# Kernel optimization log

Measured on AMD Instinct MI355X. Metric: run time of the kernel, lower is better.

Reference implementation:

```python
import jax, jax.numpy as jnp
import numpy as np

Nknn = 10
Np = 20
N = 524288
DOWN, LEFT, RIGHT, UP, WIDTH = -5.0, -5.0, 5.0, 5.0, 1.0


def setup_inputs() -> dict:
    key = jax.random.key(0)
    ks = jax.random.split(key, 20)
    def p(k, shape, fan_in):
        return jax.random.normal(k, shape, jnp.float32) / jnp.sqrt(jnp.float32(fan_in))
    inp = {
        "t": jax.random.uniform(ks[0], (1,), jnp.float32),
        "y": jax.random.normal(ks[1], (N, 4 + 2 * Np), jnp.float32),
        # net1: Linear(4,8) -> ReLU -> Linear(8,2)
        "w1a": p(ks[2], (4, 8), 4),   "b1a": p(ks[3], (8,), 4),
        "w1b": p(ks[4], (8, 2), 8),   "b1b": p(ks[5], (2,), 8),
        # net2: Linear(1,16) -> ReLU -> Linear(16,8) -> ReLU -> Linear(8,1)
        "w2a": p(ks[6], (1, 16), 1),  "b2a": p(ks[7], (16,), 1),
        "w2b": p(ks[8], (16, 8), 16), "b2b": p(ks[9], (8,), 16),
        "w2c": p(ks[10], (8, 1), 8),  "b2c": p(ks[11], (1,), 8),
        # net3: same architecture as net2
        "w3a": p(ks[12], (1, 16), 1), "b3a": p(ks[13], (16,), 1),
        "w3b": p(ks[14], (16, 8), 16),"b3b": p(ks[15], (8,), 16),
        "w3c": p(ks[16], (8, 1), 8),  "b3c": p(ks[17], (1,), 8),
    }
    return inp


def _mlp3(x, wa, ba, wb, bb, wc, bc):
    # Linear -> ReLU -> Linear -> ReLU -> Linear, applied on last axis
    h = jax.nn.relu(x @ wa + ba)
    h = jax.nn.relu(h @ wb + bb)
    return h @ wc + bc


def reference(t, y, w1a, b1a, w1b, b1b, w2a, b2a, w2b, b2b, w2c, b2c,
              w3a, b3a, w3b, b3b, w3c, b3c):
    y = y.astype(jnp.float32)
    theX = y[:, 0:2]            # positions [N,2]
    theV = y[:, 2:4]            # velocities [N,2]
    ux = y[:, 4:4 + 2 * Nknn].reshape(-1, Nknn, 2)  # neighbor offsets [N,Nknn,2]

    dxdt = theV

    # goal-attraction term f1
    door = jnp.array([RIGHT + 0.6, 0.0], jnp.float32)
    diff = door - theX
    unit_e = diff / jnp.sqrt(jnp.sum(diff * diff, axis=1, keepdims=True))
    h = jax.nn.relu(jnp.concatenate([unit_e, theV], axis=1) @ w1a + b1a)
    f1 = h @ w1b + b1b          # [N,2]

    # wall-repulsion term f2; rows inside the door gap get rightdist=100
    x0 = theX[:, 0:1]
    x1 = theX[:, 1:2]
    rightdist = jnp.where((x1 < WIDTH) & (x1 > -WIDTH), 100.0, RIGHT - x0)
    wall_in = jnp.stack([x0 - LEFT, x1 - DOWN, UP - x1, rightdist], axis=1)  # [N,4,1]
    o = _mlp3(wall_in, w2a, b2a, w2b, bb=b2b, wc=w2c, bc=b2c) if False else _mlp3(wall_in, w2a, b2a, w2b, b2b, w2c, b2c)  # [N,4,1]
    # directions: [1,0], [0,1], [0,-1], [-1,0]
    f2 = jnp.concatenate([o[:, 0] - o[:, 3], o[:, 1] - o[:, 2]], axis=1)  # [N,2]

    # neighbor-repulsion term f3 (vectorized over Nknn)
    d = jnp.sqrt(jnp.sum(ux * ux, axis=2, keepdims=True))  # [N,Nknn,1]
    f3 = -jnp.sum(_mlp3(d, w3a, b3a, w3b, b3b, w3c, b3c) * ux / d, axis=1)  # [N,2]

    dvdt = (f1 + f2 + f3) / 80.0
    dudt = jnp.zeros((y.shape[0], 2 * Nknn), y.dtype)
    result = jnp.concatenate([dxdt, dvdt, dudt], axis=1)  # [N, 4 + 2*Nknn]

    # zero out agents that have exited (x > RIGHT)
    result = jnp.where((theX[:, 0] > RIGHT)[:, None], 0.0, result)
    return result
```

## Files before the change

### kernel.cpp

```cpp
#include <hip/hip_runtime.h>

#define NROW  524288
#define BLK   256
#define NKNN  10
#define YCOLS 44
#define OCOLS 24

#define TBL    256
#define T2_LO  (-2.0f)
#define T3_LO  (0.0f)
#define T_H    (1.0f / 16.0f)
#define T_INVH 16.0f

typedef float f32x4 __attribute__((ext_vector_type(4)));

__device__ __forceinline__ float mlp_scalar_g(float s,
    const float* __restrict__ wa, const float* __restrict__ ba,
    const float* __restrict__ wb, const float* __restrict__ bb,
    const float* __restrict__ wc, const float* __restrict__ bc) {
    float h[16];
#pragma unroll
    for (int j = 0; j < 16; ++j)
        h[j] = fmaxf(fmaf(s, wa[j], ba[j]), 0.0f);
    float g[8];
#pragma unroll
    for (int k = 0; k < 8; ++k) g[k] = bb[k];
#pragma unroll
    for (int j = 0; j < 16; ++j) {
        float hj = h[j];
#pragma unroll
        for (int k = 0; k < 8; ++k)
            g[k] = fmaf(hj, wb[j * 8 + k], g[k]);
    }
    float o = bc[0];
#pragma unroll
    for (int k = 0; k < 8; ++k)
        o = fmaf(fmaxf(g[k], 0.0f), wc[k], o);
    return o;
}

__device__ __forceinline__ float tbl_eval(const float* __restrict__ T, float s, float lo) {
    float u = (s - lo) * T_INVH;
    u = fminf(fmaxf(u, 0.0f), (float)TBL - 1.001f);
    int i = (int)u;
    float f = u - (float)i;
    float va = T[i];
    float vb = T[i + 1];
    return fmaf(f, vb - va, va);
}

__global__ __launch_bounds__(BLK) void odefunc_kernel(
    const float* __restrict__ y,
    const float* __restrict__ w1a, const float* __restrict__ b1a,
    const float* __restrict__ w1b, const float* __restrict__ b1b,
    const float* __restrict__ w2a, const float* __restrict__ b2a,
    const float* __restrict__ w2b, const float* __restrict__ b2b,
    const float* __restrict__ w2c, const float* __restrict__ b2c,
    const float* __restrict__ w3a, const float* __restrict__ b3a,
    const float* __restrict__ w3b, const float* __restrict__ b3b,
    const float* __restrict__ w3c, const float* __restrict__ b3c,
    float* __restrict__ out)
{
    __shared__ f32x4 S[BLK * 6];
    __shared__ float T2v[TBL];
    __shared__ float T3v[TBL];
    __shared__ float o100s;

    const int t    = threadIdx.x;
    const int w    = t >> 6;
    const int lane = t & 63;

    const f32x4* yb = reinterpret_cast<const f32x4*>(y) + (size_t)blockIdx.x * BLK * (YCOLS / 4);
    f32x4 ld[6];
    int jj[6];
#pragma unroll
    for (int i = 0; i < 6; ++i) {
        int j  = lane + i * 64;
        int rr = j / 6;
        int cc = j - rr * 6;
        jj[i]  = j;
        ld[i]  = yb[(64 * w + rr) * 11 + cc];
    }

    T2v[t] = mlp_scalar_g(T2_LO + (float)t * T_H, w2a, b2a, w2b, b2b, w2c, b2c);
    T3v[t] = mlp_scalar_g(T3_LO + (float)t * T_H, w3a, b3a, w3b, b3b, w3c, b3c);
    if (t == 0)
        o100s = mlp_scalar_g(100.0f, w2a, b2a, w2b, b2b, w2c, b2c);

    __syncthreads();

#pragma unroll
    for (int i = 0; i < 6; ++i)
        S[384 * w + jj[i]] = ld[i];
    __builtin_amdgcn_wave_barrier();

    f32x4 a  = S[t * 6 + 0];
    f32x4 u0 = S[t * 6 + 1];
    f32x4 u1 = S[t * 6 + 2];
    f32x4 u2 = S[t * 6 + 3];
    f32x4 u3 = S[t * 6 + 4];
    f32x4 u4 = S[t * 6 + 5];
    const float o100 = o100s;

    float dx = 5.6f - a.x;
    float dy = 0.0f - a.y;
    float inv = rsqrtf(fmaf(dx, dx, dy * dy));
    float in1[4] = { dx * inv, dy * inv, a.z, a.w };
    float h1[8];
#pragma unroll
    for (int j = 0; j < 8; ++j) {
        float s = b1a[j];
#pragma unroll
        for (int k = 0; k < 4; ++k)
            s = fmaf(in1[k], w1a[k * 8 + j], s);
        h1[j] = fmaxf(s, 0.0f);
    }
    float f1x = b1b[0];
    float f1y = b1b[1];
#pragma unroll
    for (int j = 0; j < 8; ++j) {
        f1x = fmaf(h1[j], w1b[j * 2 + 0], f1x);
        f1y = fmaf(h1[j], w1b[j * 2 + 1], f1y);
    }

    bool corridor = (a.y < 1.0f) && (a.y > -1.0f);
    float o0 = tbl_eval(T2v, a.x + 5.0f, T2_LO);
    float o1 = tbl_eval(T2v, a.y + 5.0f, T2_LO);
    float o2 = tbl_eval(T2v, 5.0f - a.y, T2_LO);
    float o3 = corridor ? o100 : tbl_eval(T2v, 5.0f - a.x, T2_LO);
    float f2x = o0 - o3;
    float f2y = o1 - o2;

    float us[2 * NKNN] = { u0.x, u0.y, u0.z, u0.w,
                           u1.x, u1.y, u1.z, u1.w,
                           u2.x, u2.y, u2.z, u2.w,
                           u3.x, u3.y, u3.z, u3.w,
                           u4.x, u4.y, u4.z, u4.w };
    float f3x = 0.0f, f3y = 0.0f;
#pragma unroll
    for (int n = 0; n < NKNN; ++n) {
        float uxn = us[2 * n + 0];
        float uyn = us[2 * n + 1];
        float s2  = fmaf(uxn, uxn, uyn * uyn);
        float idn = rsqrtf(s2);
        float d   = s2 * idn;
        float m   = tbl_eval(T3v, d, T3_LO);
        float c   = m * idn;
        f3x = fmaf(-c, uxn, f3x);
        f3y = fmaf(-c, uyn, f3y);
    }

    bool dead = (a.x > 5.0f);
    const float k80 = 1.0f / 80.0f;
    f32x4 r;
    r.x = dead ? 0.0f : a.z;
    r.y = dead ? 0.0f : a.w;
    r.z = dead ? 0.0f : (f1x + f2x + f3x) * k80;
    r.w = dead ? 0.0f : (f1y + f2y + f3y) * k80;

    const f32x4 z = (f32x4)(0.0f);
    S[t * 6 + 0] = r;
    S[t * 6 + 1] = z;
    S[t * 6 + 2] = z;
    S[t * 6 + 3] = z;
    S[t * 6 + 4] = z;
    S[t * 6 + 5] = z;
    __builtin_amdgcn_wave_barrier();

    f32x4* o4 = reinterpret_cast<f32x4*>(out) + (size_t)blockIdx.x * BLK * (OCOLS / 4);
#pragma unroll
    for (int i = 0; i < 6; ++i) {
        int j = 384 * w + lane + i * 64;
        f32x4 v = S[j];
        __builtin_nontemporal_store(v, &o4[j]);
    }
}

extern "C" void kernel_launch(void* const* d_in, const int* in_sizes, int n_in,
                              void* d_out, int out_size, void* d_ws, size_t ws_size,
                              hipStream_t stream) {
    int iy = 1;
    for (int i = 0; i < n_in; ++i) {
        if (in_sizes[i] == NROW * YCOLS) { iy = i; break; }
    }
    const float* y   = (const float*)d_in[iy];
    const float* w1a = (const float*)d_in[iy + 1];
    const float* b1a = (const float*)d_in[iy + 2];
    const float* w1b = (const float*)d_in[iy + 3];
    const float* b1b = (const float*)d_in[iy + 4];
    const float* w2a = (const float*)d_in[iy + 5];
    const float* b2a = (const float*)d_in[iy + 6];
    const float* w2b = (const float*)d_in[iy + 7];
    const float* b2b = (const float*)d_in[iy + 8];
    const float* w2c = (const float*)d_in[iy + 9];
    const float* b2c = (const float*)d_in[iy + 10];
    const float* w3a = (const float*)d_in[iy + 11];
    const float* b3a = (const float*)d_in[iy + 12];
    const float* w3b = (const float*)d_in[iy + 13];
    const float* b3b = (const float*)d_in[iy + 14];
    const float* w3c = (const float*)d_in[iy + 15];
    const float* b3c = (const float*)d_in[iy + 16];
    float* out = (float*)d_out;

    hipLaunchKernelGGL(odefunc_kernel, dim3(NROW / BLK), dim3(BLK), 0, stream,
                       y, w1a, b1a, w1b, b1b,
                       w2a, b2a, w2b, b2b, w2c, b2c,
                       w3a, b3a, w3b, b3b, w3c, b3c, out);
}
```

Measured before the change: 30.48 us.

## Process two row tiles per block and prefetch the second during compute

Each block now handles two 256-row tiles instead of one, halving the grid. The per-block table build (two MLP lookup tables plus the o100 value) is amortized over twice as many rows. The second tile's global load is issued before computing the first tile, overlapping memory latency with compute. The cost is fewer blocks in flight and more registers held for the prefetched tile, which may reduce occupancy.

```diff
diff --git a/kernel.cpp b/kernel.cpp
--- a/kernel.cpp
+++ b/kernel.cpp
@@ -2,6 +2,7 @@
 
 #define NROW  524288
 #define BLK   256
+#define TPB   2
 #define NKNN  10
 #define YCOLS 44
 #define OCOLS 24
@@ -47,6 +48,112 @@
     float va = T[i];
     float vb = T[i + 1];
     return fmaf(f, vb - va, va);
+}
+
+__device__ __forceinline__ void load_tile(const f32x4* __restrict__ yb,
+                                          int w, int lane, f32x4 ld[6]) {
+#pragma unroll
+    for (int i = 0; i < 6; ++i) {
+        int j  = lane + i * 64;
+        int rr = j / 6;
+        int cc = j - rr * 6;
+        ld[i]  = yb[(64 * w + rr) * 11 + cc];
+    }
+}
+
+__device__ __forceinline__ void stage_tile(f32x4* __restrict__ S,
+                                           int w, int lane, const f32x4 ld[6]) {
+#pragma unroll
+    for (int i = 0; i < 6; ++i)
+        S[384 * w + lane + i * 64] = ld[i];
+}
+
+__device__ __forceinline__ void compute_row(f32x4* __restrict__ S, int t,
+    const float* __restrict__ T2v, const float* __restrict__ T3v, float o100,
+    const float* __restrict__ w1a, const float* __restrict__ b1a,
+    const float* __restrict__ w1b, const float* __restrict__ b1b)
+{
+    f32x4 a  = S[t * 6 + 0];
+    f32x4 u0 = S[t * 6 + 1];
+    f32x4 u1 = S[t * 6 + 2];
+    f32x4 u2 = S[t * 6 + 3];
+    f32x4 u3 = S[t * 6 + 4];
+    f32x4 u4 = S[t * 6 + 5];
+
+    float dx = 5.6f - a.x;
+    float dy = 0.0f - a.y;
+    float inv = rsqrtf(fmaf(dx, dx, dy * dy));
+    float in1[4] = { dx * inv, dy * inv, a.z, a.w };
+    float h1[8];
+#pragma unroll
+    for (int j = 0; j < 8; ++j) {
+        float s = b1a[j];
+#pragma unroll
+        for (int k = 0; k < 4; ++k)
+            s = fmaf(in1[k], w1a[k * 8 + j], s);
+        h1[j] = fmaxf(s, 0.0f);
+    }
+    float f1x = b1b[0];
+    float f1y = b1b[1];
+#pragma unroll
+    for (int j = 0; j < 8; ++j) {
+        f1x = fmaf(h1[j], w1b[j * 2 + 0], f1x);
+        f1y = fmaf(h1[j], w1b[j * 2 + 1], f1y);
+    }
+
+    bool corridor = (a.y < 1.0f) && (a.y > -1.0f);
+    float o0 = tbl_eval(T2v, a.x + 5.0f, T2_LO);
+    float o1 = tbl_eval(T2v, a.y + 5.0f, T2_LO);
+    float o2 = tbl_eval(T2v, 5.0f - a.y, T2_LO);
+    float o3 = corridor ? o100 : tbl_eval(T2v, 5.0f - a.x, T2_LO);
+    float f2x = o0 - o3;
+    float f2y = o1 - o2;
+
+    float us[2 * NKNN] = { u0.x, u0.y, u0.z, u0.w,
+                           u1.x, u1.y, u1.z, u1.w,
+                           u2.x, u2.y, u2.z, u2.w,
+                           u3.x, u3.y, u3.z, u3.w,
+                           u4.x, u4.y, u4.z, u4.w };
+    float f3x = 0.0f, f3y = 0.0f;
+#pragma unroll
+    for (int n = 0; n < NKNN; ++n) {
+        float uxn = us[2 * n + 0];
+        float uyn = us[2 * n + 1];
+        float s2  = fmaf(uxn, uxn, uyn * uyn);
+        float idn = rsqrtf(s2);
+        float d   = s2 * idn;
+        float m   = tbl_eval(T3v, d, T3_LO);
+        float c   = m * idn;
+        f3x = fmaf(-c, uxn, f3x);
+        f3y = fmaf(-c, uyn, f3y);
+    }
+
+    bool dead = (a.x > 5.0f);
+    const float k80 = 1.0f / 80.0f;
+    f32x4 r;
+    r.x = dead ? 0.0f : a.z;
+    r.y = dead ? 0.0f : a.w;
+    r.z = dead ? 0.0f : (f1x + f2x + f3x) * k80;
+    r.w = dead ? 0.0f : (f1y + f2y + f3y) * k80;
+
+    const f32x4 z = (f32x4)(0.0f);
+    S[t * 6 + 0] = r;
+    S[t * 6 + 1] = z;
+    S[t * 6 + 2] = z;
+    S[t * 6 + 3] = z;
+    S[t * 6 + 4] = z;
+    S[t * 6 + 5] = z;
+}
+
+__device__ __forceinline__ void store_tile(f32x4* __restrict__ ob,
+                                           const f32x4* __restrict__ S,
+                                           int w, int lane) {
+#pragma unroll
+    for (int i = 0; i < 6; ++i) {
+        int j = 384 * w + lane + i * 64;
+        f32x4 v = S[j];
+        __builtin_nontemporal_store(v, &ob[j]);
+    }
 }
 
 __global__ __launch_bounds__(BLK) void odefunc_kernel(
@@ -70,17 +177,15 @@
     const int w    = t >> 6;
     const int lane = t & 63;
 
-    const f32x4* yb = reinterpret_cast<const f32x4*>(y) + (size_t)blockIdx.x * BLK * (YCOLS / 4);
-    f32x4 ld[6];
-    int jj[6];
-#pragma unroll
-    for (int i = 0; i < 6; ++i) {
-        int j  = lane + i * 64;
-        int rr = j / 6;
-        int cc = j - rr * 6;
-        jj[i]  = j;
-        ld[i]  = yb[(64 * w + rr) * 11 + cc];
-    }
+    const f32x4* yb0 = reinterpret_cast<const f32x4*>(y)
+                     + (size_t)blockIdx.x * TPB * BLK * (YCOLS / 4);
+    const f32x4* yb1 = yb0 + BLK * (YCOLS / 4);
+    f32x4* ob0 = reinterpret_cast<f32x4*>(out)
+               + (size_t)blockIdx.x * TPB * BLK * (OCOLS / 4);
+    f32x4* ob1 = ob0 + BLK * (OCOLS / 4);
+
+    f32x4 ld0[6];
+    load_tile(yb0, w, lane, ld0);
 
     T2v[t] = mlp_scalar_g(T2_LO + (float)t * T_H, w2a, b2a, w2b, b2b, w2c, b2c);
     T3v[t] = mlp_scalar_g(T3_LO + (float)t * T_H, w3a, b3a, w3b, b3b, w3c, b3c);
@@ -88,92 +193,25 @@
         o100s = mlp_scalar_g(100.0f, w2a, b2a, w2b, b2b, w2c, b2c);
 
     __syncthreads();
-
-#pragma unroll
-    for (int i = 0; i < 6; ++i)
-        S[384 * w + jj[i]] = ld[i];
-    __builtin_amdgcn_wave_barrier();
-
-    f32x4 a  = S[t * 6 + 0];
-    f32x4 u0 = S[t * 6 + 1];
-    f32x4 u1 = S[t * 6 + 2];
-    f32x4 u2 = S[t * 6 + 3];
-    f32x4 u3 = S[t * 6 + 4];
-    f32x4 u4 = S[t * 6 + 5];
     const float o100 = o100s;
 
-    float dx = 5.6f - a.x;
-    float dy = 0.0f - a.y;
-    float inv = rsqrtf(fmaf(dx, dx, dy * dy));
-    float in1[4] = { dx * inv, dy * inv, a.z, a.w };
-    float h1[8];
-#pragma unroll
-    for (int j = 0; j < 8; ++j) {
-        float s = b1a[j];
-#pragma unroll
-        for (int k = 0; k < 4; ++k)
-            s = fmaf(in1[k], w1a[k * 8 + j], s);
-        h1[j] = fmaxf(s, 0.0f);
-    }
-    float f1x = b1b[0];
-    float f1y = b1b[1];
-#pragma unroll
-    for (int j = 0; j < 8; ++j) {
-        f1x = fmaf(h1[j], w1b[j * 2 + 0], f1x);
-        f1y = fmaf(h1[j], w1b[j * 2 + 1], f1y);
-    }
-
-    bool corridor = (a.y < 1.0f) && (a.y > -1.0f);
-    float o0 = tbl_eval(T2v, a.x + 5.0f, T2_LO);
-    float o1 = tbl_eval(T2v, a.y + 5.0f, T2_LO);
-    float o2 = tbl_eval(T2v, 5.0f - a.y, T2_LO);
-    float o3 = corridor ? o100 : tbl_eval(T2v, 5.0f - a.x, T2_LO);
-    float f2x = o0 - o3;
-    float f2y = o1 - o2;
-
-    float us[2 * NKNN] = { u0.x, u0.y, u0.z, u0.w,
-                           u1.x, u1.y, u1.z, u1.w,
-                           u2.x, u2.y, u2.z, u2.w,
-                           u3.x, u3.y, u3.z, u3.w,
-                           u4.x, u4.y, u4.z, u4.w };
-    float f3x = 0.0f, f3y = 0.0f;
-#pragma unroll
-    for (int n = 0; n < NKNN; ++n) {
-        float uxn = us[2 * n + 0];
-        float uyn = us[2 * n + 1];
-        float s2  = fmaf(uxn, uxn, uyn * uyn);
-        float idn = rsqrtf(s2);
-        float d   = s2 * idn;
-        float m   = tbl_eval(T3v, d, T3_LO);
-        float c   = m * idn;
-        f3x = fmaf(-c, uxn, f3x);
-        f3y = fmaf(-c, uyn, f3y);
-    }
-
-    bool dead = (a.x > 5.0f);
-    const float k80 = 1.0f / 80.0f;
-    f32x4 r;
-    r.x = dead ? 0.0f : a.z;
-    r.y = dead ? 0.0f : a.w;
-    r.z = dead ? 0.0f : (f1x + f2x + f3x) * k80;
-    r.w = dead ? 0.0f : (f1y + f2y + f3y) * k80;
-
-    const f32x4 z = (f32x4)(0.0f);
-    S[t * 6 + 0] = r;
-    S[t * 6 + 1] = z;
-    S[t * 6 + 2] = z;
-    S[t * 6 + 3] = z;
-    S[t * 6 + 4] = z;
-    S[t * 6 + 5] = z;
-    __builtin_amdgcn_wave_barrier();
-
-    f32x4* o4 = reinterpret_cast<f32x4*>(out) + (size_t)blockIdx.x * BLK * (OCOLS / 4);
-#pragma unroll
-    for (int i = 0; i < 6; ++i) {
-        int j = 384 * w + lane + i * 64;
-        f32x4 v = S[j];
-        __builtin_nontemporal_store(v, &o4[j]);
-    }
+    stage_tile(S, w, lane, ld0);
+    __builtin_amdgcn_wave_barrier();
+
+    f32x4 ld1[6];
+    load_tile(yb1, w, lane, ld1);
+
+    compute_row(S, t, T2v, T3v, o100, w1a, b1a, w1b, b1b);
+    __builtin_amdgcn_wave_barrier();
+    store_tile(ob0, S, w, lane);
+    __builtin_amdgcn_wave_barrier();
+
+    stage_tile(S, w, lane, ld1);
+    __builtin_amdgcn_wave_barrier();
+
+    compute_row(S, t, T2v, T3v, o100, w1a, b1a, w1b, b1b);
+    __builtin_amdgcn_wave_barrier();
+    store_tile(ob1, S, w, lane);
 }
 
 extern "C" void kernel_launch(void* const* d_in, const int* in_sizes, int n_in,
@@ -202,7 +240,7 @@
     const float* b3c = (const float*)d_in[iy + 16];
     float* out = (float*)d_out;
 
-    hipLaunchKernelGGL(odefunc_kernel, dim3(NROW / BLK), dim3(BLK), 0, stream,
+    hipLaunchKernelGGL(odefunc_kernel, dim3(NROW / (BLK * TPB)), dim3(BLK), 0, stream,
                        y, w1a, b1a, w1b, b1b,
                        w2a, b2a, w2b, b2b, w2c, b2c,
                        w3a, b3a, w3b, b3b, w3c, b3c, out);
```

Result: faster. 28.57 us (-6.3%).
